# Performance work log

Hardware: AMD Instinct MI355X
Metric: run time of the kernel (lower is better)

The kernel has to match this reference:

```python
import jax, jax.numpy as jnp
import numpy as np

B, C_IN, C_OUT, H, W = 32, 256, 256, 32, 32


def setup_inputs() -> dict:
    key = jax.random.key(0)
    kx, kw, kb = jax.random.split(key, 3)
    x = jax.random.normal(kx, (B, C_IN, H, W), dtype=jnp.float32)
    # 1x1 conv == pointwise linear over channels: weight [out_c, in_c], bias [out_c]
    conv_w = jax.random.normal(kw, (C_OUT, C_IN), dtype=jnp.float32) * (1.0 / np.sqrt(C_IN))
    conv_b = jax.random.normal(kb, (C_OUT,), dtype=jnp.float32) * 0.01
    return {"x": x, "conv_w": conv_w, "conv_b": conv_b}


def reference(x, conv_w, conv_b):
    b, c, h, w = x.shape
    hw = h * w
    q = x.reshape(b, c, hw)  # q == k == flattened x
    # score[b,i,j] = sum_c q[b,c,i] * q[b,c,j]  -> (b, hw, hw)
    score = jnp.einsum('bci,bcj->bij', q, q)
    attn = jax.nn.softmax(score, axis=-1)
    # 1x1 conv V projection: (b, out_c, h, w)
    v = jnp.einsum('oc,bchw->bohw', conv_w, x) + conv_b[None, :, None, None]
    v = v.reshape(b, -1, hw).transpose(0, 2, 1)  # (b, hw, out_c)
    out = jnp.einsum('bij,bjo->bio', attn, v)  # (b, hw, out_c)
    # torch does .transpose(-1,-1) (a no-op) then reshape(b,-1,h,w) in row-major
    out = out.reshape(b, -1, h, w)  # (b, out_c, h, w), position-major flatten as in torch
    # MaxPool2d(2): 2x2 windows, stride 2
    oc = out.shape[1]
    out = out.reshape(b, oc, h // 2, 2, w // 2, 2).max(axis=(3, 5))
    return out
```

## Files before the change

### kernel.cpp

```cpp
#include <hip/hip_runtime.h>
#include <math.h>

#define BB 32
#define CC 256
#define NN 1024
#define KSTR 264
#define PSTR 40
#define THR 8.0f

typedef unsigned short u16;
typedef u16 u16x8 __attribute__((ext_vector_type(8)));
typedef _Float16 h16;
typedef h16 h16x8 __attribute__((ext_vector_type(8)));
typedef h16 h16x4 __attribute__((ext_vector_type(4)));
typedef float f32x4 __attribute__((ext_vector_type(4)));

__device__ __forceinline__ h16x8 ldh8(const u16* p) {
    return __builtin_bit_cast(h16x8, *(const u16x8*)p);
}
__device__ __forceinline__ f32x4 mfma16(h16x8 a, h16x8 b, f32x4 c) {
    return __builtin_amdgcn_mfma_f32_16x16x32_f16(a, b, c, 0, 0, 0);
}

__global__ __launch_bounds__(256) void k_wprep(const float* __restrict__ w,
                                               u16* __restrict__ whf) {
    int s = blockIdx.x * 256 + threadIdx.x;
    int ot = s >> 9, ks = (s >> 6) & 7, l = s & 63;
    const float* src = w + (size_t)(ot * 16 + (l & 15)) * CC + ks * 32 + 8 * (l >> 4);
    float4 a = *(const float4*)src;
    float4 c = *(const float4*)(src + 4);
    u16x8 o;
    o[0] = __builtin_bit_cast(u16, (h16)a.x); o[1] = __builtin_bit_cast(u16, (h16)a.y);
    o[2] = __builtin_bit_cast(u16, (h16)a.z); o[3] = __builtin_bit_cast(u16, (h16)a.w);
    o[4] = __builtin_bit_cast(u16, (h16)c.x); o[5] = __builtin_bit_cast(u16, (h16)c.y);
    o[6] = __builtin_bit_cast(u16, (h16)c.z); o[7] = __builtin_bit_cast(u16, (h16)c.w);
    *(u16x8*)(whf + (size_t)s * 8) = o;
}

__global__ __launch_bounds__(256) void k_split(const float* __restrict__ x,
                                               u16* __restrict__ qf) {
    __shared__ float lds[64][65];
    int bid = blockIdx.x;
    int b = bid >> 6, ct = (bid >> 4) & 3, pt = bid & 15;
    int t = threadIdx.x;
    int c0 = ct * 64, p0 = pt * 64;
    const float* xb = x + ((size_t)b * CC + c0) * NN + p0;
#pragma unroll
    for (int it = 0; it < 4; ++it) {
        int cl = (t >> 4) + it * 16;
        int pl = (t & 15) * 4;
        float4 v = *(const float4*)(xb + (size_t)cl * NN + pl);
        lds[pl + 0][cl] = v.x;
        lds[pl + 1][cl] = v.y;
        lds[pl + 2][cl] = v.z;
        lds[pl + 3][cl] = v.w;
    }
    __syncthreads();
    u16* qb = qf + ((size_t)b * NN + p0) * CC + c0;
#pragma unroll
    for (int it = 0; it < 2; ++it) {
        int pl = (t >> 3) + it * 32;
        int cl = (t & 7) * 8;
        u16x8 hv;
#pragma unroll
        for (int e = 0; e < 8; ++e) hv[e] = __builtin_bit_cast(u16, (h16)lds[pl][cl + e]);
        *(u16x8*)(qb + (size_t)pl * CC + cl) = hv;
    }
}

__global__ __launch_bounds__(256, 2) void k_vgemm(const u16* __restrict__ qf,
                                                  const u16* __restrict__ whf,
                                                  const float* __restrict__ bias,
                                                  u16* __restrict__ vf) {
    __shared__ __align__(16) u16 smem[18432];
    int bid = blockIdx.x;
    int b = bid >> 4, pt = bid & 15;
    int t = threadIdx.x;
    int wave = t >> 6, lane = t & 63;
    int l15 = lane & 15, l4 = lane >> 4;
    int p0 = pt * 64, o0 = wave * 64;

#pragma unroll
    for (int it = 0; it < 8; ++it) {
        int sidx = t + it * 256;
        int row = sidx >> 5, ch = (sidx & 31) * 8;
        *(u16x8*)&smem[row * KSTR + ch] =
            *(const u16x8*)(qf + ((size_t)b * NN + p0 + row) * CC + ch);
    }
    __syncthreads();

    f32x4 acc[4][4];
#pragma unroll
    for (int m = 0; m < 4; ++m)
#pragma unroll
        for (int n = 0; n < 4; ++n) acc[m][n] = (f32x4){0.f, 0.f, 0.f, 0.f};
#pragma unroll
    for (int ks = 0; ks < 8; ++ks) {
        h16x8 afr[4], bfr[4];
#pragma unroll
        for (int m = 0; m < 4; ++m)
            afr[m] = ldh8(whf + (size_t)(((wave * 4 + m) * 8 + ks) * 64 + lane) * 8);
#pragma unroll
        for (int n = 0; n < 4; ++n)
            bfr[n] = ldh8(&smem[(n * 16 + l15) * KSTR + ks * 32 + 8 * l4]);
#pragma unroll
        for (int m = 0; m < 4; ++m)
#pragma unroll
            for (int n = 0; n < 4; ++n) acc[m][n] = mfma16(afr[m], bfr[n], acc[m][n]);
    }
    __syncthreads();

    u16* Vs = smem + wave * 4608;
#pragma unroll
    for (int m = 0; m < 4; ++m) {
#pragma unroll
        for (int r = 0; r < 4; ++r) {
            int ol = m * 16 + 4 * l4 + r;
            float bv = bias[o0 + ol];
#pragma unroll
            for (int n = 0; n < 4; ++n)
                Vs[ol * 72 + n * 16 + l15] =
                    __builtin_bit_cast(u16, (h16)(acc[m][n][r] + bv));
        }
    }
#pragma unroll
    for (int m = 0; m < 4; ++m) {
#pragma unroll
        for (int jtl = 0; jtl < 2; ++jtl) {
            u16x8 v = *(u16x8*)&Vs[(m * 16 + l15) * 72 + jtl * 32 + 8 * l4];
            size_t idx = (((size_t)b * 32 + pt * 2 + jtl) * 16 + wave * 4 + m) * 512 +
                         lane * 8;
            *(u16x8*)(vf + idx) = v;
        }
    }
}

#define SMEM_BYTES 39424
__global__ __launch_bounds__(256, 2) void k_attn(const u16* __restrict__ qf,
                                                 const u16* __restrict__ vf,
                                                 float* __restrict__ out) {
    __shared__ __align__(16) char smem[SMEM_BYTES];
    u16* Kt = (u16*)smem;
    u16* Pt = (u16*)(smem + 33792);
    float* Sc = (float*)(smem + 38912);

    int bid = blockIdx.x;
    int xcd = bid & 7, s0 = bid >> 3;
    int b = xcd * 4 + (s0 >> 4);
    int iblk = s0 & 15;
    int i0 = iblk * 64;
    int t = threadIdx.x;
    int wave = t >> 6, lane = t & 63;
    int l15 = lane & 15, l4 = lane >> 4;
    int iw = i0 + wave * 16;

    const u16* qb = qf + (size_t)b * NN * CC;
    const u16* vfb = vf + (size_t)b * (32 * 16 * 512);

    h16x8 qfr[8];
#pragma unroll
    for (int ks = 0; ks < 8; ++ks)
        qfr[ks] = ldh8(qb + (size_t)(iw + l15) * CC + ks * 32 + 8 * l4);

    f32x4 oacc[16];
#pragma unroll
    for (int i = 0; i < 16; ++i) oacc[i] = (f32x4){0.f, 0.f, 0.f, 0.f};
    float m = -INFINITY, l = 0.f;

    {
        u16x8 kp[4];
#pragma unroll
        for (int p = 0; p < 4; ++p) {
            int sidx = t + p * 256;
            kp[p] = *(const u16x8*)(qb + (size_t)(sidx >> 5) * CC + (sidx & 31) * 8);
        }
#pragma unroll
        for (int p = 0; p < 4; ++p) {
            int sidx = t + p * 256;
            *(u16x8*)&Kt[(sidx >> 5) * KSTR + (sidx & 31) * 8] = kp[p];
        }
    }
    __syncthreads();

    u16* Pw = Pt + wave * 16 * PSTR;
    float* Scw = Sc + wave * 16;

    for (int jt = 0; jt < 32; ++jt) {
        int cur = jt & 1;
        int j0 = jt * 32;
        const u16* Kc = Kt + cur * (32 * KSTR) + l15 * KSTR + 8 * l4;

        u16x8 vfr[16];
#pragma unroll
        for (int of = 0; of < 16; ++of)
            vfr[of] = *(const u16x8*)(vfb + ((size_t)(jt * 16 + of) * 512 + lane * 8));

        u16x8 kp[4];
        if (jt < 31) {
#pragma unroll
            for (int p = 0; p < 4; ++p) {
                int sidx = t + p * 256;
                kp[p] = *(const u16x8*)(qb + (size_t)(j0 + 32 + (sidx >> 5)) * CC +
                                        (sidx & 31) * 8);
            }
        }

        f32x4 s0v = (f32x4){0.f, 0.f, 0.f, 0.f};
        f32x4 s1v = (f32x4){0.f, 0.f, 0.f, 0.f};
#pragma unroll
        for (int ks = 0; ks < 8; ++ks) {
            h16x8 a0 = ldh8(Kc + ks * 32);
            h16x8 a1 = ldh8(Kc + 16 * KSTR + ks * 32);
            s0v = mfma16(a0, qfr[ks], s0v);
            s1v = mfma16(a1, qfr[ks], s1v);
        }

        float mx = fmaxf(fmaxf(fmaxf(s0v[0], s0v[1]), fmaxf(s0v[2], s0v[3])),
                         fmaxf(fmaxf(s1v[0], s1v[1]), fmaxf(s1v[2], s1v[3])));
        mx = fmaxf(mx, __shfl_xor(mx, 16));
        mx = fmaxf(mx, __shfl_xor(mx, 32));
        if (__any(mx > m + THR)) {
            float mnew = fmaxf(m, mx);
            float sc = __expf(m - mnew);
            m = mnew;
            l *= sc;
            Scw[l15] = sc;
            f32x4 s4 = *(f32x4*)&Scw[4 * l4];
#pragma unroll
            for (int of = 0; of < 16; ++of)
#pragma unroll
                for (int r = 0; r < 4; ++r) oacc[of][r] *= s4[r];
        }
        float p0 = __expf(s0v[0] - m), p1 = __expf(s0v[1] - m);
        float p2 = __expf(s0v[2] - m), p3 = __expf(s0v[3] - m);
        float p4 = __expf(s1v[0] - m), p5 = __expf(s1v[1] - m);
        float p6 = __expf(s1v[2] - m), p7 = __expf(s1v[3] - m);
        float rs = ((p0 + p1) + (p2 + p3)) + ((p4 + p5) + (p6 + p7));
        rs += __shfl_xor(rs, 16);
        rs += __shfl_xor(rs, 32);
        l += rs;

        h16x4 pk0 = {(h16)p0, (h16)p1, (h16)p2, (h16)p3};
        h16x4 pk1 = {(h16)p4, (h16)p5, (h16)p6, (h16)p7};
        *(h16x4*)(Pw + l15 * PSTR + 4 * l4) = pk0;
        *(h16x4*)(Pw + l15 * PSTR + 16 + 4 * l4) = pk1;
        h16x8 pa = ldh8(Pw + l15 * PSTR + 8 * l4);

#pragma unroll
        for (int of = 0; of < 16; ++of)
            oacc[of] = mfma16(pa, __builtin_bit_cast(h16x8, vfr[of]), oacc[of]);

        if (jt < 31) {
#pragma unroll
            for (int p = 0; p < 4; ++p) {
                int sidx = t + p * 256;
                *(u16x8*)&Kt[(cur ^ 1) * (32 * KSTR) + (sidx >> 5) * KSTR +
                             (sidx & 31) * 8] = kp[p];
            }
            __syncthreads();
        }
    }

    {
        float inv = 1.0f / l;
        Scw[l15] = inv;
        f32x4 inv4 = *(f32x4*)&Scw[4 * l4];
#pragma unroll
        for (int of = 0; of < 16; ++of)
#pragma unroll
            for (int r = 0; r < 4; ++r) oacc[of][r] *= inv4[r];
    }

    float* Old = (float*)smem;
#pragma unroll
    for (int half = 0; half < 2; ++half) {
        __syncthreads();
        if ((wave >> 1) == half) {
            int wrow = (wave & 1) * 16;
#pragma unroll
            for (int of = 0; of < 16; ++of)
#pragma unroll
                for (int r = 0; r < 4; ++r)
                    Old[(wrow + 4 * l4 + r) * 260 + of * 16 + l15] = oacc[of][r];
        }
        __syncthreads();
#pragma unroll
        for (int it = 0; it < 8; ++it) {
            int q = it * 16 + (t >> 4);
            int ill = q >> 2, pl = q & 3, pw = t & 15;
            const float* row = &Old[ill * 260];
            int ob = pl * 64 + pw * 2;
            float mx = fmaxf(fmaxf(row[ob], row[ob + 1]),
                             fmaxf(row[ob + 32], row[ob + 33]));
            int i = i0 + half * 32 + ill;
            out[(((size_t)b * CC + (i >> 2)) * 16 + (i & 3) * 4 + pl) * 16 + pw] = mx;
        }
    }
}

extern "C" void kernel_launch(void* const* d_in, const int* in_sizes, int n_in,
                              void* d_out, int out_size, void* d_ws, size_t ws_size,
                              hipStream_t stream) {
    const float* x = (const float*)d_in[0];
    const float* w = (const float*)d_in[1];
    const float* bias = (const float*)d_in[2];
    float* out = (float*)d_out;
    u16* qf = (u16*)d_ws;
    u16* vf = qf + (size_t)BB * NN * CC;
    u16* whf = vf + (size_t)BB * NN * CC;
    k_wprep<<<32, 256, 0, stream>>>(w, whf);
    k_split<<<2048, 256, 0, stream>>>(x, qf);
    k_vgemm<<<512, 256, 0, stream>>>(qf, whf, bias, vf);
    k_attn<<<512, 256, 0, stream>>>(qf, vf, out);
}
```

Before: 147.6 us.

## Rewrite attention with 32x32 MFMA, split-KV waves, and direct global-to-LDS loads

The attention kernel now uses 32x32x16 MFMA tiles and splits the key range across two wave groups, merging their partial softmax states at the end. K and V tiles are staged into XOR-swizzled LDS with global_load_lds. P is kept in registers and rearranged with permlane32 swaps instead of a round trip through LDS. The weight-prep kernel is folded into the split kernel, and the V GEMM uses smaller tiles at higher occupancy with swizzled direct LDS loads. The aim is fewer launches, fewer LDS bank conflicts, less register-LDS traffic and better MFMA throughput, at the cost of more complex synchronisation and a cross-wave merge step.

```diff
diff --git a/kernel.cpp b/kernel.cpp
--- a/kernel.cpp
+++ b/kernel.cpp
@@ -4,16 +4,17 @@
 #define BB 32
 #define CC 256
 #define NN 1024
-#define KSTR 264
-#define PSTR 40
 #define THR 8.0f
 
 typedef unsigned short u16;
+typedef unsigned int u32;
 typedef u16 u16x8 __attribute__((ext_vector_type(8)));
 typedef _Float16 h16;
+typedef h16 h16x2 __attribute__((ext_vector_type(2)));
 typedef h16 h16x8 __attribute__((ext_vector_type(8)));
-typedef h16 h16x4 __attribute__((ext_vector_type(4)));
 typedef float f32x4 __attribute__((ext_vector_type(4)));
+typedef float f32x16 __attribute__((ext_vector_type(16)));
+typedef u32 u32x4v __attribute__((ext_vector_type(4)));
 
 __device__ __forceinline__ h16x8 ldh8(const u16* p) {
     return __builtin_bit_cast(h16x8, *(const u16x8*)p);
@@ -21,28 +22,36 @@
 __device__ __forceinline__ f32x4 mfma16(h16x8 a, h16x8 b, f32x4 c) {
     return __builtin_amdgcn_mfma_f32_16x16x32_f16(a, b, c, 0, 0, 0);
 }
-
-__global__ __launch_bounds__(256) void k_wprep(const float* __restrict__ w,
+__device__ __forceinline__ f32x16 mfma32(h16x8 a, h16x8 b, f32x16 c) {
+    return __builtin_amdgcn_mfma_f32_32x32x16_f16(a, b, c, 0, 0, 0);
+}
+__device__ __forceinline__ void gll16(const void* g, void* l) {
+    __builtin_amdgcn_global_load_lds((const __attribute__((address_space(1))) u32*)g,
+                                     (__attribute__((address_space(3))) u32*)l, 16, 0, 0);
+}
+
+__global__ __launch_bounds__(256) void k_split(const float* __restrict__ x,
+                                               u16* __restrict__ qf,
+                                               const float* __restrict__ w,
                                                u16* __restrict__ whf) {
-    int s = blockIdx.x * 256 + threadIdx.x;
-    int ot = s >> 9, ks = (s >> 6) & 7, l = s & 63;
-    const float* src = w + (size_t)(ot * 16 + (l & 15)) * CC + ks * 32 + 8 * (l >> 4);
-    float4 a = *(const float4*)src;
-    float4 c = *(const float4*)(src + 4);
-    u16x8 o;
-    o[0] = __builtin_bit_cast(u16, (h16)a.x); o[1] = __builtin_bit_cast(u16, (h16)a.y);
-    o[2] = __builtin_bit_cast(u16, (h16)a.z); o[3] = __builtin_bit_cast(u16, (h16)a.w);
-    o[4] = __builtin_bit_cast(u16, (h16)c.x); o[5] = __builtin_bit_cast(u16, (h16)c.y);
-    o[6] = __builtin_bit_cast(u16, (h16)c.z); o[7] = __builtin_bit_cast(u16, (h16)c.w);
-    *(u16x8*)(whf + (size_t)s * 8) = o;
-}
-
-__global__ __launch_bounds__(256) void k_split(const float* __restrict__ x,
-                                               u16* __restrict__ qf) {
     __shared__ float lds[64][65];
     int bid = blockIdx.x;
+    int t = threadIdx.x;
+    if (bid >= 2048) {
+        int s = (bid - 2048) * 256 + t;
+        int ot = s >> 9, ks = (s >> 6) & 7, l = s & 63;
+        const float* src = w + (size_t)(ot * 16 + (l & 15)) * CC + ks * 32 + 8 * (l >> 4);
+        float4 a = *(const float4*)src;
+        float4 c = *(const float4*)(src + 4);
+        u16x8 o;
+        o[0] = __builtin_bit_cast(u16, (h16)a.x); o[1] = __builtin_bit_cast(u16, (h16)a.y);
+        o[2] = __builtin_bit_cast(u16, (h16)a.z); o[3] = __builtin_bit_cast(u16, (h16)a.w);
+        o[4] = __builtin_bit_cast(u16, (h16)c.x); o[5] = __builtin_bit_cast(u16, (h16)c.y);
+        o[6] = __builtin_bit_cast(u16, (h16)c.z); o[7] = __builtin_bit_cast(u16, (h16)c.w);
+        *(u16x8*)(whf + (size_t)s * 8) = o;
+        return;
+    }
     int b = bid >> 6, ct = (bid >> 4) & 3, pt = bid & 15;
-    int t = threadIdx.x;
     int c0 = ct * 64, p0 = pt * 64;
     const float* xb = x + ((size_t)b * CC + c0) * NN + p0;
 #pragma unroll
@@ -68,49 +77,50 @@
     }
 }
 
-__global__ __launch_bounds__(256, 2) void k_vgemm(const u16* __restrict__ qf,
+__global__ __launch_bounds__(256, 4) void k_vgemm(const u16* __restrict__ qf,
                                                   const u16* __restrict__ whf,
                                                   const float* __restrict__ bias,
-                                                  u16* __restrict__ vf) {
-    __shared__ __align__(16) u16 smem[18432];
+                                                  u16* __restrict__ vimg) {
+    __shared__ __align__(16) u16 smem[10240];
     int bid = blockIdx.x;
-    int b = bid >> 4, pt = bid & 15;
-    int t = threadIdx.x;
-    int wave = t >> 6, lane = t & 63;
+    int b = bid >> 5, pt = bid & 31;
+    int t = threadIdx.x, wave = t >> 6, lane = t & 63;
     int l15 = lane & 15, l4 = lane >> 4;
-    int p0 = pt * 64, o0 = wave * 64;
-
-#pragma unroll
-    for (int it = 0; it < 8; ++it) {
-        int sidx = t + it * 256;
-        int row = sidx >> 5, ch = (sidx & 31) * 8;
-        *(u16x8*)&smem[row * KSTR + ch] =
-            *(const u16x8*)(qf + ((size_t)b * NN + p0 + row) * CC + ch);
-    }
-    __syncthreads();
-
-    f32x4 acc[4][4];
+    int p0 = pt * 32, o0 = wave * 64;
+    {
+        int Gb = wave * 256;
+#pragma unroll
+        for (int inst = 0; inst < 4; ++inst) {
+            int G = Gb + inst * 64 + lane;
+            int row = G >> 5, g = G & 31;
+            gll16(qf + (size_t)(b * NN + p0 + row) * CC + ((g ^ (row & 7)) << 3),
+                  smem + (size_t)(Gb + inst * 64) * 8);
+        }
+    }
+    __syncthreads();
+    f32x4 acc[4][2];
 #pragma unroll
     for (int m = 0; m < 4; ++m)
 #pragma unroll
-        for (int n = 0; n < 4; ++n) acc[m][n] = (f32x4){0.f, 0.f, 0.f, 0.f};
+        for (int n = 0; n < 2; ++n) acc[m][n] = (f32x4){0.f, 0.f, 0.f, 0.f};
 #pragma unroll
     for (int ks = 0; ks < 8; ++ks) {
-        h16x8 afr[4], bfr[4];
+        h16x8 afr[4], bfr[2];
 #pragma unroll
         for (int m = 0; m < 4; ++m)
             afr[m] = ldh8(whf + (size_t)(((wave * 4 + m) * 8 + ks) * 64 + lane) * 8);
 #pragma unroll
-        for (int n = 0; n < 4; ++n)
-            bfr[n] = ldh8(&smem[(n * 16 + l15) * KSTR + ks * 32 + 8 * l4]);
+        for (int n = 0; n < 2; ++n) {
+            int row = n * 16 + l15;
+            bfr[n] = ldh8(smem + row * 256 + (((4 * ks + l4) ^ (l15 & 7)) << 3));
+        }
 #pragma unroll
         for (int m = 0; m < 4; ++m)
 #pragma unroll
-            for (int n = 0; n < 4; ++n) acc[m][n] = mfma16(afr[m], bfr[n], acc[m][n]);
-    }
-    __syncthreads();
-
-    u16* Vs = smem + wave * 4608;
+            for (int n = 0; n < 2; ++n) acc[m][n] = mfma16(afr[m], bfr[n], acc[m][n]);
+    }
+    __syncthreads();
+    u16* Vs = smem + wave * 2560;
 #pragma unroll
     for (int m = 0; m < 4; ++m) {
 #pragma unroll
@@ -118,182 +128,210 @@
             int ol = m * 16 + 4 * l4 + r;
             float bv = bias[o0 + ol];
 #pragma unroll
-            for (int n = 0; n < 4; ++n)
-                Vs[ol * 72 + n * 16 + l15] =
+            for (int n = 0; n < 2; ++n)
+                Vs[ol * 40 + n * 16 + l15] =
                     __builtin_bit_cast(u16, (h16)(acc[m][n][r] + bv));
         }
     }
 #pragma unroll
     for (int m = 0; m < 4; ++m) {
-#pragma unroll
-        for (int jtl = 0; jtl < 2; ++jtl) {
-            u16x8 v = *(u16x8*)&Vs[(m * 16 + l15) * 72 + jtl * 32 + 8 * l4];
-            size_t idx = (((size_t)b * 32 + pt * 2 + jtl) * 16 + wave * 4 + m) * 512 +
-                         lane * 8;
-            *(u16x8*)(vf + idx) = v;
-        }
-    }
-}
-
-#define SMEM_BYTES 39424
+        u16x8 v = *(u16x8*)&Vs[(m * 16 + l15) * 40 + 8 * l4];
+        *(u16x8*)(vimg + ((size_t)(b * 32 + pt) * 256 + o0 + m * 16 + l15) * 32 + 8 * l4) = v;
+    }
+}
+
+#define SMEM_A 66560
 __global__ __launch_bounds__(256, 2) void k_attn(const u16* __restrict__ qf,
-                                                 const u16* __restrict__ vf,
+                                                 const u16* __restrict__ vimg,
                                                  float* __restrict__ out) {
-    __shared__ __align__(16) char smem[SMEM_BYTES];
-    u16* Kt = (u16*)smem;
-    u16* Pt = (u16*)(smem + 33792);
-    float* Sc = (float*)(smem + 38912);
+    __shared__ __align__(16) char smem[SMEM_A];
+    u16* Kb = (u16*)smem;
+    u16* Vb = (u16*)(smem + 32768);
+    float* Mx = (float*)(smem + 65536);
+    float* Lx = (float*)(smem + 66048);
+    float* Ob = (float*)smem;
 
     int bid = blockIdx.x;
     int xcd = bid & 7, s0 = bid >> 3;
     int b = xcd * 4 + (s0 >> 4);
-    int iblk = s0 & 15;
-    int i0 = iblk * 64;
-    int t = threadIdx.x;
-    int wave = t >> 6, lane = t & 63;
-    int l15 = lane & 15, l4 = lane >> 4;
-    int iw = i0 + wave * 16;
-
+    int i0 = (s0 & 15) * 64;
+    int t = threadIdx.x, wave = t >> 6, lane = t & 63;
+    int rg = wave & 1, jg = wave >> 1;
+    int l31 = lane & 31, lh = lane >> 5, l7 = lane & 7;
     const u16* qb = qf + (size_t)b * NN * CC;
-    const u16* vfb = vf + (size_t)b * (32 * 16 * 512);
-
-    h16x8 qfr[8];
-#pragma unroll
-    for (int ks = 0; ks < 8; ++ks)
-        qfr[ks] = ldh8(qb + (size_t)(iw + l15) * CC + ks * 32 + 8 * l4);
-
-    f32x4 oacc[16];
-#pragma unroll
-    for (int i = 0; i < 16; ++i) oacc[i] = (f32x4){0.f, 0.f, 0.f, 0.f};
+    const u16* vtb = vimg + (size_t)b * (32 * 8192);
+
+    {
+        int Gb = wave * 512;
+#pragma unroll
+        for (int inst = 0; inst < 8; ++inst) {
+            int G = Gb + inst * 64 + lane;
+            int row = (G >> 5) & 31, g = G & 31, tile = G >> 10;
+            gll16(qb + (size_t)(i0 + tile * 32 + row) * CC + ((g ^ (row & 7)) << 3),
+                  Kb + (size_t)(Gb + inst * 64) * 8);
+        }
+    }
+    __syncthreads();
+    h16x8 qfr[16];
+    {
+        const u16* qB = Kb + rg * 8192 + l31 * 256;
+#pragma unroll
+        for (int ks = 0; ks < 16; ++ks)
+            qfr[ks] = ldh8(qB + (((2 * ks + lh) ^ l7) << 3));
+    }
+    __syncthreads();
+    {
+        int Gb = wave * 512;
+#pragma unroll
+        for (int inst = 0; inst < 8; ++inst) {
+            int G = Gb + inst * 64 + lane;
+            int row = (G >> 5) & 31, g = G & 31, tile = G >> 10;
+            gll16(qb + (size_t)((tile * 16) * 32 + row) * CC + ((g ^ (row & 7)) << 3),
+                  Kb + (size_t)(Gb + inst * 64) * 8);
+        }
+#pragma unroll
+        for (int inst = 0; inst < 8; ++inst) {
+            int G = Gb + inst * 64 + lane;
+            int row = (G >> 2) & 255, gi = G & 3, tile = G >> 10;
+            gll16(vtb + (size_t)(tile * 16) * 8192 + row * 32 + ((gi ^ ((row >> 1) & 3)) << 3),
+                  Vb + (size_t)(Gb + inst * 64) * 8);
+        }
+    }
+    __syncthreads();
+
+    f32x16 oacc[8];
+#pragma unroll
+    for (int oc = 0; oc < 8; ++oc)
+#pragma unroll
+        for (int r = 0; r < 16; ++r) oacc[oc][r] = 0.f;
     float m = -INFINITY, l = 0.f;
-
-    {
-        u16x8 kp[4];
-#pragma unroll
-        for (int p = 0; p < 4; ++p) {
-            int sidx = t + p * 256;
-            kp[p] = *(const u16x8*)(qb + (size_t)(sidx >> 5) * CC + (sidx & 31) * 8);
-        }
-#pragma unroll
-        for (int p = 0; p < 4; ++p) {
-            int sidx = t + p * 256;
-            *(u16x8*)&Kt[(sidx >> 5) * KSTR + (sidx & 31) * 8] = kp[p];
-        }
-    }
-    __syncthreads();
-
-    u16* Pw = Pt + wave * 16 * PSTR;
-    float* Scw = Sc + wave * 16;
-
-    for (int jt = 0; jt < 32; ++jt) {
-        int cur = jt & 1;
-        int j0 = jt * 32;
-        const u16* Kc = Kt + cur * (32 * KSTR) + l15 * KSTR + 8 * l4;
-
-        u16x8 vfr[16];
-#pragma unroll
-        for (int of = 0; of < 16; ++of)
-            vfr[of] = *(const u16x8*)(vfb + ((size_t)(jt * 16 + of) * 512 + lane * 8));
-
-        u16x8 kp[4];
-        if (jt < 31) {
-#pragma unroll
-            for (int p = 0; p < 4; ++p) {
-                int sidx = t + p * 256;
-                kp[p] = *(const u16x8*)(qb + (size_t)(j0 + 32 + (sidx >> 5)) * CC +
-                                        (sidx & 31) * 8);
-            }
-        }
-
-        f32x4 s0v = (f32x4){0.f, 0.f, 0.f, 0.f};
-        f32x4 s1v = (f32x4){0.f, 0.f, 0.f, 0.f};
-#pragma unroll
-        for (int ks = 0; ks < 8; ++ks) {
-            h16x8 a0 = ldh8(Kc + ks * 32);
-            h16x8 a1 = ldh8(Kc + 16 * KSTR + ks * 32);
-            s0v = mfma16(a0, qfr[ks], s0v);
-            s1v = mfma16(a1, qfr[ks], s1v);
-        }
-
-        float mx = fmaxf(fmaxf(fmaxf(s0v[0], s0v[1]), fmaxf(s0v[2], s0v[3])),
-                         fmaxf(fmaxf(s1v[0], s1v[1]), fmaxf(s1v[2], s1v[3])));
-        mx = fmaxf(mx, __shfl_xor(mx, 16));
+    const u16* KbJ = Kb + jg * 8192;
+    const u16* VbJ = Vb + jg * 8192;
+    int l31s = (l31 >> 1) & 3;
+
+    for (int it = 0; it < 16; ++it) {
+        f32x16 s;
+#pragma unroll
+        for (int r = 0; r < 16; ++r) s[r] = 0.f;
+        __builtin_amdgcn_s_setprio(1);
+#pragma unroll
+        for (int ks = 0; ks < 16; ++ks) {
+            h16x8 a = ldh8(KbJ + l31 * 256 + (((2 * ks + lh) ^ l7) << 3));
+            s = mfma32(a, qfr[ks], s);
+        }
+        __builtin_amdgcn_s_setprio(0);
+        __syncthreads();
+        if (it < 15) {
+            int Gb = wave * 512;
+#pragma unroll
+            for (int inst = 0; inst < 8; ++inst) {
+                int G = Gb + inst * 64 + lane;
+                int row = (G >> 5) & 31, g = G & 31, tile = G >> 10;
+                gll16(qb + (size_t)((tile * 16 + it + 1) * 32 + row) * CC +
+                          ((g ^ (row & 7)) << 3),
+                      Kb + (size_t)(Gb + inst * 64) * 8);
+            }
+        }
+        float mx = s[0];
+#pragma unroll
+        for (int r = 1; r < 16; ++r) mx = fmaxf(mx, s[r]);
         mx = fmaxf(mx, __shfl_xor(mx, 32));
         if (__any(mx > m + THR)) {
-            float mnew = fmaxf(m, mx);
-            float sc = __expf(m - mnew);
-            m = mnew;
-            l *= sc;
-            Scw[l15] = sc;
-            f32x4 s4 = *(f32x4*)&Scw[4 * l4];
-#pragma unroll
-            for (int of = 0; of < 16; ++of)
-#pragma unroll
-                for (int r = 0; r < 4; ++r) oacc[of][r] *= s4[r];
-        }
-        float p0 = __expf(s0v[0] - m), p1 = __expf(s0v[1] - m);
-        float p2 = __expf(s0v[2] - m), p3 = __expf(s0v[3] - m);
-        float p4 = __expf(s1v[0] - m), p5 = __expf(s1v[1] - m);
-        float p6 = __expf(s1v[2] - m), p7 = __expf(s1v[3] - m);
-        float rs = ((p0 + p1) + (p2 + p3)) + ((p4 + p5) + (p6 + p7));
-        rs += __shfl_xor(rs, 16);
+            float mn = fmaxf(m, mx);
+            float f = __expf(m - mn);
+            m = mn;
+            l *= f;
+#pragma unroll
+            for (int oc = 0; oc < 8; ++oc)
+#pragma unroll
+                for (int r = 0; r < 16; ++r) oacc[oc][r] *= f;
+        }
+        float p[16], rs = 0.f;
+#pragma unroll
+        for (int r = 0; r < 16; ++r) { p[r] = __expf(s[r] - m); rs += p[r]; }
         rs += __shfl_xor(rs, 32);
         l += rs;
-
-        h16x4 pk0 = {(h16)p0, (h16)p1, (h16)p2, (h16)p3};
-        h16x4 pk1 = {(h16)p4, (h16)p5, (h16)p6, (h16)p7};
-        *(h16x4*)(Pw + l15 * PSTR + 4 * l4) = pk0;
-        *(h16x4*)(Pw + l15 * PSTR + 16 + 4 * l4) = pk1;
-        h16x8 pa = ldh8(Pw + l15 * PSTR + 8 * l4);
-
-#pragma unroll
-        for (int of = 0; of < 16; ++of)
-            oacc[of] = mfma16(pa, __builtin_bit_cast(h16x8, vfr[of]), oacc[of]);
-
-        if (jt < 31) {
-#pragma unroll
-            for (int p = 0; p < 4; ++p) {
-                int sidx = t + p * 256;
-                *(u16x8*)&Kt[(cur ^ 1) * (32 * KSTR) + (sidx >> 5) * KSTR +
-                             (sidx & 31) * 8] = kp[p];
-            }
-            __syncthreads();
-        }
-    }
-
-    {
-        float inv = 1.0f / l;
-        Scw[l15] = inv;
-        f32x4 inv4 = *(f32x4*)&Scw[4 * l4];
-#pragma unroll
-        for (int of = 0; of < 16; ++of)
-#pragma unroll
-            for (int r = 0; r < 4; ++r) oacc[of][r] *= inv4[r];
-    }
-
-    float* Old = (float*)smem;
-#pragma unroll
-    for (int half = 0; half < 2; ++half) {
+        u32 pk0 = __builtin_bit_cast(u32, __builtin_amdgcn_cvt_pkrtz(p[0], p[1]));
+        u32 pk1 = __builtin_bit_cast(u32, __builtin_amdgcn_cvt_pkrtz(p[2], p[3]));
+        u32 pk2 = __builtin_bit_cast(u32, __builtin_amdgcn_cvt_pkrtz(p[4], p[5]));
+        u32 pk3 = __builtin_bit_cast(u32, __builtin_amdgcn_cvt_pkrtz(p[6], p[7]));
+        u32 pk4 = __builtin_bit_cast(u32, __builtin_amdgcn_cvt_pkrtz(p[8], p[9]));
+        u32 pk5 = __builtin_bit_cast(u32, __builtin_amdgcn_cvt_pkrtz(p[10], p[11]));
+        u32 pk6 = __builtin_bit_cast(u32, __builtin_amdgcn_cvt_pkrtz(p[12], p[13]));
+        u32 pk7 = __builtin_bit_cast(u32, __builtin_amdgcn_cvt_pkrtz(p[14], p[15]));
+        asm volatile("v_permlane32_swap_b32 %0, %1" : "+v"(pk0), "+v"(pk2));
+        asm volatile("v_permlane32_swap_b32 %0, %1" : "+v"(pk1), "+v"(pk3));
+        asm volatile("v_permlane32_swap_b32 %0, %1" : "+v"(pk4), "+v"(pk6));
+        asm volatile("v_permlane32_swap_b32 %0, %1" : "+v"(pk5), "+v"(pk7));
+        h16x8 pa0 = __builtin_bit_cast(h16x8, (u32x4v){pk0, pk1, pk2, pk3});
+        h16x8 pa1 = __builtin_bit_cast(h16x8, (u32x4v){pk4, pk5, pk6, pk7});
+        __builtin_amdgcn_s_setprio(1);
+#pragma unroll
+        for (int oc = 0; oc < 8; ++oc) {
+            h16x8 v0 = ldh8(VbJ + (oc * 32 + l31) * 32 + (((0 + lh) ^ l31s) << 3));
+            h16x8 v1 = ldh8(VbJ + (oc * 32 + l31) * 32 + (((2 + lh) ^ l31s) << 3));
+            oacc[oc] = mfma32(v0, pa0, oacc[oc]);
+            oacc[oc] = mfma32(v1, pa1, oacc[oc]);
+        }
+        __builtin_amdgcn_s_setprio(0);
         __syncthreads();
-        if ((wave >> 1) == half) {
-            int wrow = (wave & 1) * 16;
-#pragma unroll
-            for (int of = 0; of < 16; ++of)
-#pragma unroll
-                for (int r = 0; r < 4; ++r)
-                    Old[(wrow + 4 * l4 + r) * 260 + of * 16 + l15] = oacc[of][r];
-        }
-        __syncthreads();
-#pragma unroll
-        for (int it = 0; it < 8; ++it) {
-            int q = it * 16 + (t >> 4);
-            int ill = q >> 2, pl = q & 3, pw = t & 15;
-            const float* row = &Old[ill * 260];
-            int ob = pl * 64 + pw * 2;
-            float mx = fmaxf(fmaxf(row[ob], row[ob + 1]),
-                             fmaxf(row[ob + 32], row[ob + 33]));
-            int i = i0 + half * 32 + ill;
-            out[(((size_t)b * CC + (i >> 2)) * 16 + (i & 3) * 4 + pl) * 16 + pw] = mx;
+        if (it < 15) {
+            int Gb = wave * 512;
+#pragma unroll
+            for (int inst = 0; inst < 8; ++inst) {
+                int G = Gb + inst * 64 + lane;
+                int row = (G >> 2) & 255, gi = G & 3, tile = G >> 10;
+                gll16(vtb + (size_t)(tile * 16 + it + 1) * 8192 + row * 32 +
+                          ((gi ^ ((row >> 1) & 3)) << 3),
+                      Vb + (size_t)(Gb + inst * 64) * 8);
+            }
+        }
+    }
+
+    if (lane < 32) {
+        Mx[wave * 32 + l31] = m;
+        Lx[wave * 32 + l31] = l;
+    }
+    if (jg == 1) {
+#pragma unroll
+        for (int oc = 0; oc < 8; ++oc)
+#pragma unroll
+            for (int q = 0; q < 4; ++q) {
+                f32x4 v = (f32x4){oacc[oc][4 * q + 0], oacc[oc][4 * q + 1],
+                                  oacc[oc][4 * q + 2], oacc[oc][4 * q + 3]};
+                *(f32x4*)&Ob[(((rg * 8 + oc) * 4 + q) * 64 + lane) * 4] = v;
+            }
+    }
+    __syncthreads();
+    if (jg == 0) {
+        int pidx = (wave ^ 2) * 32 + l31;
+        float m2 = Mx[pidx], l2 = Lx[pidx];
+        float ms = fmaxf(m, m2);
+        float f0 = __expf(m - ms), f1 = __expf(m2 - ms);
+        float inv = 1.f / (l * f0 + l2 * f1);
+        f0 *= inv; f1 *= inv;
+#pragma unroll
+        for (int oc = 0; oc < 8; ++oc)
+#pragma unroll
+            for (int q = 0; q < 4; ++q) {
+                f32x4 o1 = *(const f32x4*)&Ob[(((rg * 8 + oc) * 4 + q) * 64 + lane) * 4];
+#pragma unroll
+                for (int e = 0; e < 4; ++e)
+                    oacc[oc][4 * q + e] = oacc[oc][4 * q + e] * f0 + o1[e] * f1;
+            }
+        int I = i0 + rg * 32 + l31;
+        float* ob = out + ((size_t)(b * 256 + (I >> 2)) * 16 + (I & 3) * 4) * 16;
+#pragma unroll
+        for (int pl = 0; pl < 4; ++pl) {
+#pragma unroll
+            for (int pwh = 0; pwh < 8; ++pwh) {
+                int r0 = 2 * (pwh & 1) + 4 * (pwh >> 1);
+                int oc0 = 2 * pl;
+                float v = fmaxf(fmaxf(oacc[oc0][r0], oacc[oc0][r0 + 1]),
+                                fmaxf(oacc[oc0 + 1][r0], oacc[oc0 + 1][r0 + 1]));
+                int pw = (pwh & 1) + 4 * (pwh >> 1) + 2 * lh;
+                ob[pl * 16 + pw] = v;
+            }
         }
     }
 }
@@ -306,10 +344,9 @@
     const float* bias = (const float*)d_in[2];
     float* out = (float*)d_out;
     u16* qf = (u16*)d_ws;
-    u16* vf = qf + (size_t)BB * NN * CC;
-    u16* whf = vf + (size_t)BB * NN * CC;
-    k_wprep<<<32, 256, 0, stream>>>(w, whf);
-    k_split<<<2048, 256, 0, stream>>>(x, qf);
-    k_vgemm<<<512, 256, 0, stream>>>(qf, whf, bias, vf);
-    k_attn<<<512, 256, 0, stream>>>(qf, vf, out);
-}
+    u16* vimg = qf + (size_t)BB * NN * CC;
+    u16* whf = vimg + (size_t)BB * NN * CC;
+    k_split<<<2080, 256, 0, stream>>>(x, qf, w, whf);
+    k_vgemm<<<1024, 256, 0, stream>>>(qf, whf, bias, vimg);
+    k_attn<<<512, 256, 0, stream>>>(qf, vimg, out);
+}
```

Result: slower. 172.9 us (+17.1%).
